# Kernel tuning notes

Measured on AMD Instinct MI355X. Metric: run time of the kernel, lower is better.

## Reference

```python
import jax, jax.numpy as jnp
import numpy as np

HIDDEN = 20


def setup_inputs() -> dict:
    key = jax.random.key(0)
    ks = jax.random.split(key, 8)
    B, T = 8192, 2048
    x = jax.random.normal(ks[0], (B, T), dtype=jnp.float32)
    # linear1: 1 -> HIDDEN
    W1 = jax.random.normal(ks[1], (HIDDEN, 1), dtype=jnp.float32) * 0.5
    b1 = jax.random.normal(ks[2], (HIDDEN,), dtype=jnp.float32) * 0.1
    # LSTMCell(HIDDEN, HIDDEN): torch layout [4*H, H], gate order i,f,g,o
    W_ih = jax.random.normal(ks[3], (4 * HIDDEN, HIDDEN), dtype=jnp.float32) * 0.2
    W_hh = jax.random.normal(ks[4], (4 * HIDDEN, HIDDEN), dtype=jnp.float32) * 0.2
    b_ih = jax.random.normal(ks[5], (4 * HIDDEN,), dtype=jnp.float32) * 0.1
    b_hh = jax.random.normal(ks[6], (4 * HIDDEN,), dtype=jnp.float32) * 0.1
    # linear2: HIDDEN -> 1
    W2 = jax.random.normal(ks[7], (1, HIDDEN), dtype=jnp.float32) * 0.2
    b2 = jnp.zeros((1,), dtype=jnp.float32)
    return {"input": x, "W1": W1, "b1": b1, "W_ih": W_ih, "W_hh": W_hh,
            "b_ih": b_ih, "b_hh": b_hh, "W2": W2, "b2": b2}


def reference(input, W1, b1, W_ih, W_hh, b_ih, b_hh, W2, b2):
    B, T = input.shape
    h0 = jnp.zeros((B, HIDDEN), dtype=input.dtype)
    c0 = jnp.zeros((B, HIDDEN), dtype=input.dtype)

    def step(carry, x_t):
        h, c = carry
        # linear1 on scalar input: [B] -> [B, HIDDEN]
        hid = x_t[:, None] * W1[:, 0][None, :] + b1
        # LSTMCell gates, torch order: i, f, g, o
        gates = hid @ W_ih.T + b_ih + h @ W_hh.T + b_hh  # [B, 4H]
        i_g, f_g, g_g, o_g = jnp.split(gates, 4, axis=-1)
        c_new = jax.nn.sigmoid(f_g) * c + jax.nn.sigmoid(i_g) * jnp.tanh(g_g)
        h_new = jax.nn.sigmoid(o_g) * jnp.tanh(c_new)
        out = h_new @ W2.T + b2  # [B, 1]
        return (h_new, c_new), out[:, 0]

    xs = input.T  # [T, B]
    _, outs = jax.lax.scan(step, (h0, c0), xs)  # outs: [T, B]
    return outs.T  # [B, T]
```

## Files before the change

kernel.cpp:

```cpp
#include <hip/hip_runtime.h>


#define HID 20
#define ROWS_PER_WAVE 3
#define NTHREADS 64
#define L2E 1.4426950408889634f

typedef float v2f __attribute__((ext_vector_type(2)));

__device__ __forceinline__ float exp2_hw(float v) { return __builtin_amdgcn_exp2f(v); }
__device__ __forceinline__ float rcp_hw(float v)  { return __builtin_amdgcn_rcpf(v); }

__device__ __forceinline__ float sig_s(float gs) {
    return rcp_hw(1.0f + exp2_hw(-gs));
}
__device__ __forceinline__ float tanh_2Ls(float gs2) {
    return (2.0f * L2E) - (4.0f * L2E) * rcp_hw(1.0f + exp2_hw(gs2));
}
__device__ __forceinline__ float tanh_c(float cs) {
    return 1.0f - 2.0f * rcp_hw(1.0f + exp2_hw(cs));
}

__global__ __attribute__((amdgpu_flat_work_group_size(NTHREADS, NTHREADS),
                          amdgpu_waves_per_eu(3, 3)))
void lstm_wave(
        const float* __restrict__ x,
        const float* __restrict__ W1,
        const float* __restrict__ b1,
        const float* __restrict__ W_ih,
        const float* __restrict__ W_hh,
        const float* __restrict__ b_ih,
        const float* __restrict__ b_hh,
        const float* __restrict__ W2,
        const float* __restrict__ b2,
        float* __restrict__ out,
        const int B, const int T)
{
    const int lane = threadIdx.x;
    const int lrow = lane / HID;
    const int m    = lane % HID;
    const bool outlane = (lrow == 3) && (m < ROWS_PER_WAVE);
    const int rslot = (lrow == 3) ? m : lrow;
    const long rowbase = (long)blockIdx.x * ROWS_PER_WAVE;
    const long row = rowbase + ((lrow == 3) ? (long)((m < 3) ? m : 0) : (long)lrow);
    const long arow = (row < B) ? row : (B - 1);
    const bool ovalid = outlane && (row < B);

    __shared__ __align__(16) float hbuf[2][ROWS_PER_WAVE + 1][HID];

    float u[4], v[4];
    if (lrow < 3) {
#pragma unroll
        for (int g = 0; g < 4; ++g) {
            const int j = g * HID + m;
            const float s = (g == 2) ? (2.0f * L2E) : L2E;
            float uu = 0.f, vv = 0.f;
#pragma unroll
            for (int k = 0; k < HID; ++k) {
                const float wi = W_ih[j * HID + k];
                uu += wi * W1[k];
                vv += wi * b1[k];
            }
            u[g] = s * uu;
            v[g] = s * (vv + b_ih[j] + b_hh[j]);
        }
    } else {
#pragma unroll
        for (int g = 0; g < 4; ++g) { u[g] = 0.f; v[g] = 0.f; }
        v[0] = b2[0];
    }

    v2f whh2[4][HID / 2];
    if (lrow < 3) {
#pragma unroll
        for (int g = 0; g < 4; ++g) {
            const int j = g * HID + m;
            const float s = (g == 2) ? (2.0f * L2E) : L2E;
#pragma unroll
            for (int kk = 0; kk < HID / 2; ++kk) {
                v2f w;
                w.x = s * W_hh[j * HID + 2 * kk];
                w.y = s * W_hh[j * HID + 2 * kk + 1];
                whh2[g][kk] = w;
            }
        }
    } else {
#pragma unroll
        for (int kk = 0; kk < HID / 2; ++kk) {
            v2f w; w.x = W2[2 * kk]; w.y = W2[2 * kk + 1];
            whh2[0][kk] = w;
            whh2[1][kk] = (v2f)(0.f);
            whh2[2][kk] = (v2f)(0.f);
            whh2[3][kk] = (v2f)(0.f);
        }
    }

#pragma unroll
    for (int g = 0; g < 4; ++g)
#pragma unroll
        for (int kk = 0; kk < HID / 2; ++kk)
            asm volatile("" : "+v"(whh2[g][kk]));

    float cs = 0.f;
    hbuf[0][lrow][m] = 0.f;
    hbuf[1][lrow][m] = 0.f;
    __syncthreads();

    const float* __restrict__ xrow = x   + arow * T;
    float* __restrict__       orow = out + arow * T;

    const float4* __restrict__ rd0 = (const float4*)&hbuf[0][rslot][0];
    const float4* __restrict__ rd1 = (const float4*)&hbuf[1][rslot][0];
    float* __restrict__ wr0 = &hbuf[1][lrow][m];
    float* __restrict__ wr1 = &hbuf[0][lrow][m];

    float xv_next = xrow[0];

#define GATE_BODY(RD, WR, OUT_IDX_VALID, OUT_IDX)                               \
    {                                                                            \
        v2f a0, a1, a2, a3;                                                      \
        a0.x = v[0] + xv * u[0]; a0.y = 0.f;                                     \
        a1.x = v[1] + xv * u[1]; a1.y = 0.f;                                     \
        a2.x = v[2] + xv * u[2]; a2.y = 0.f;                                     \
        a3.x = v[3] + xv * u[3]; a3.y = 0.f;                                     \
        _Pragma("unroll")                                                        \
        for (int q = 0; q < 5; ++q) {                                            \
            const float4 f = RD[q];                                              \
            v2f hA; hA.x = f.x; hA.y = f.y;                                      \
            v2f hB; hB.x = f.z; hB.y = f.w;                                      \
            a0 = __builtin_elementwise_fma(whh2[0][2*q],   hA, a0);              \
            a1 = __builtin_elementwise_fma(whh2[1][2*q],   hA, a1);              \
            a2 = __builtin_elementwise_fma(whh2[2][2*q],   hA, a2);              \
            a3 = __builtin_elementwise_fma(whh2[3][2*q],   hA, a3);              \
            a0 = __builtin_elementwise_fma(whh2[0][2*q+1], hB, a0);              \
            a1 = __builtin_elementwise_fma(whh2[1][2*q+1], hB, a1);              \
            a2 = __builtin_elementwise_fma(whh2[2][2*q+1], hB, a2);              \
            a3 = __builtin_elementwise_fma(whh2[3][2*q+1], hB, a3);              \
        }                                                                        \
        const float g0 = a0.x + a0.y;                                            \
        const float g1 = a1.x + a1.y;                                            \
        const float g2 = a2.x + a2.y;                                            \
        const float g3 = a3.x + a3.y;                                            \
        if ((OUT_IDX_VALID) && ovalid) orow[OUT_IDX] = g0;                       \
        const float ig  = sig_s(g0);                                             \
        const float fg  = sig_s(g1);                                             \
        const float ggs = tanh_2Ls(g2);                                          \
        const float og  = sig_s(g3);                                             \
        cs = fg * cs + ig * ggs;                                                 \
        *(WR) = og * tanh_c(cs);                                                 \
        __syncthreads();                                                         \
    }

    for (int t = 0; t < T; t += 2) {
        {
            const float xv = xv_next;
            xv_next = xrow[t + 1];
            GATE_BODY(rd0, wr0, t > 0, t - 1)
        }
        {
            const float xv = xv_next;
            const int tn = (t + 2 < T) ? (t + 2) : (T - 1);
            xv_next = xrow[tn];
            GATE_BODY(rd1, wr1, true, t)
        }
    }

    if (ovalid) {
        float o = v[0];
#pragma unroll
        for (int q = 0; q < 5; ++q) {
            const float4 f = rd0[q];
            o += whh2[0][2*q].x   * f.x + whh2[0][2*q].y   * f.y
               + whh2[0][2*q+1].x * f.z + whh2[0][2*q+1].y * f.w;
        }
        orow[T - 1] = o;
    }
#undef GATE_BODY
}

extern "C" void kernel_launch(void* const* d_in, const int* in_sizes, int n_in,
                              void* d_out, int out_size, void* d_ws, size_t ws_size,
                              hipStream_t stream) {
    (void)n_in; (void)d_ws; (void)ws_size; (void)out_size;
    const float* x    = (const float*)d_in[0];
    const float* W1   = (const float*)d_in[1];
    const float* b1   = (const float*)d_in[2];
    const float* W_ih = (const float*)d_in[3];
    const float* W_hh = (const float*)d_in[4];
    const float* b_ih = (const float*)d_in[5];
    const float* b_hh = (const float*)d_in[6];
    const float* W2   = (const float*)d_in[7];
    const float* b2   = (const float*)d_in[8];
    float* out        = (float*)d_out;

    const int B = 8192;
    const int T = in_sizes[0] / B;
    const int grid = (B + ROWS_PER_WAVE - 1) / ROWS_PER_WAVE;

    lstm_wave<<<grid, NTHREADS, 0, stream>>>(x, W1, b1, W_ih, W_hh, b_ih, b_hh, W2, b2, out, B, T);
}
```

Baseline: 1.180 ms.

## Process two independent row groups per wave to reuse W_hh registers

Each wave now advances six batch rows, two groups of three, instead of three, so every lane runs two interleaved LSTM recurrences with the same register-resident W_hh weights. This halves the grid, doubles independent FMA and transcendental work between barriers to hide latency, and spreads the per-step barrier cost over twice as many rows. The waves-per-EU hint drops from 3 to 2 to make room for the extra registers, which lowers occupancy.

After: 1.521 ms. 28.9% more time.

```diff
diff --git a/kernel.cpp b/kernel.cpp
--- a/kernel.cpp
+++ b/kernel.cpp
@@ -2,7 +2,8 @@
 
 
 #define HID 20
-#define ROWS_PER_WAVE 3
+#define RPG 3
+#define ROWS_PER_WAVE 6
 #define NTHREADS 64
 #define L2E 1.4426950408889634f
 
@@ -22,7 +23,7 @@
 }
 
 __global__ __attribute__((amdgpu_flat_work_group_size(NTHREADS, NTHREADS),
-                          amdgpu_waves_per_eu(3, 3)))
+                          amdgpu_waves_per_eu(2, 2)))
 void lstm_wave(
         const float* __restrict__ x,
         const float* __restrict__ W1,
@@ -39,17 +40,23 @@
     const int lane = threadIdx.x;
     const int lrow = lane / HID;
     const int m    = lane % HID;
-    const bool outlane = (lrow == 3) && (m < ROWS_PER_WAVE);
-    const int rslot = (lrow == 3) ? m : lrow;
+    const bool gatelane = (lane < 60);
+    const bool outlane  = (lrow == 3) && (m < RPG);
+    const int rA = gatelane ? lrow : (outlane ? m : 0);
     const long rowbase = (long)blockIdx.x * ROWS_PER_WAVE;
-    const long row = rowbase + ((lrow == 3) ? (long)((m < 3) ? m : 0) : (long)lrow);
-    const long arow = (row < B) ? row : (B - 1);
-    const bool ovalid = outlane && (row < B);
-
-    __shared__ __align__(16) float hbuf[2][ROWS_PER_WAVE + 1][HID];
+    const long rowA = rowbase + rA;
+    const long rowB = rowA + RPG;
+    const long aA = (rowA < B) ? rowA : (long)(B - 1);
+    const long aB = (rowB < B) ? rowB : (long)(B - 1);
+    const bool ovA = outlane && (rowA < B);
+    const bool ovB = outlane && (rowB < B);
+    const int rsA = gatelane ? lrow : (outlane ? m : 6);
+    const int rsB = gatelane ? (lrow + 3) : (outlane ? (m + 3) : 7);
+
+    __shared__ __align__(16) float hbuf[2][8][HID];
 
     float u[4], v[4];
-    if (lrow < 3) {
+    if (gatelane) {
 #pragma unroll
         for (int g = 0; g < 4; ++g) {
             const int j = g * HID + m;
@@ -71,7 +78,7 @@
     }
 
     v2f whh2[4][HID / 2];
-    if (lrow < 3) {
+    if (gatelane) {
 #pragma unroll
         for (int g = 0; g < 4; ++g) {
             const int j = g * HID + m;
@@ -101,81 +108,131 @@
         for (int kk = 0; kk < HID / 2; ++kk)
             asm volatile("" : "+v"(whh2[g][kk]));
 
-    float cs = 0.f;
-    hbuf[0][lrow][m] = 0.f;
-    hbuf[1][lrow][m] = 0.f;
+    float csA = 0.f, csB = 0.f;
+    if (gatelane) {
+        hbuf[0][lrow][m] = 0.f;  hbuf[0][lrow + 3][m] = 0.f;
+        hbuf[1][lrow][m] = 0.f;  hbuf[1][lrow + 3][m] = 0.f;
+    }
     __syncthreads();
 
-    const float* __restrict__ xrow = x   + arow * T;
-    float* __restrict__       orow = out + arow * T;
-
-    const float4* __restrict__ rd0 = (const float4*)&hbuf[0][rslot][0];
-    const float4* __restrict__ rd1 = (const float4*)&hbuf[1][rslot][0];
-    float* __restrict__ wr0 = &hbuf[1][lrow][m];
-    float* __restrict__ wr1 = &hbuf[0][lrow][m];
-
-    float xv_next = xrow[0];
-
-#define GATE_BODY(RD, WR, OUT_IDX_VALID, OUT_IDX)                               \
+    const float* __restrict__ xrowA = x + aA * T;
+    const float* __restrict__ xrowB = x + aB * T;
+    float* __restrict__ orowA = out + aA * T;
+    float* __restrict__ orowB = out + aB * T;
+
+    const float4* __restrict__ rdA0 = (const float4*)&hbuf[0][rsA][0];
+    const float4* __restrict__ rdA1 = (const float4*)&hbuf[1][rsA][0];
+    const float4* __restrict__ rdB0 = (const float4*)&hbuf[0][rsB][0];
+    const float4* __restrict__ rdB1 = (const float4*)&hbuf[1][rsB][0];
+    float* __restrict__ wrA0 = &hbuf[1][lrow][m];
+    float* __restrict__ wrB0 = &hbuf[1][(lrow + 3) & 7][m];
+    float* __restrict__ wrA1 = &hbuf[0][lrow][m];
+    float* __restrict__ wrB1 = &hbuf[0][(lrow + 3) & 7][m];
+
+    float xA_next = xrowA[0];
+    float xB_next = xrowB[0];
+
+#define STEP_BODY(RDA, RDB, WRA, WRB, OUTVALID_PREV, OUT_IDX)                    \
     {                                                                            \
-        v2f a0, a1, a2, a3;                                                      \
-        a0.x = v[0] + xv * u[0]; a0.y = 0.f;                                     \
-        a1.x = v[1] + xv * u[1]; a1.y = 0.f;                                     \
-        a2.x = v[2] + xv * u[2]; a2.y = 0.f;                                     \
-        a3.x = v[3] + xv * u[3]; a3.y = 0.f;                                     \
+        v2f qa0, qa1, qa2, qa3, qb0, qb1, qb2, qb3;                              \
+        qa0.x = v[0] + xA * u[0]; qa0.y = 0.f;                                   \
+        qa1.x = v[1] + xA * u[1]; qa1.y = 0.f;                                   \
+        qa2.x = v[2] + xA * u[2]; qa2.y = 0.f;                                   \
+        qa3.x = v[3] + xA * u[3]; qa3.y = 0.f;                                   \
+        qb0.x = v[0] + xB * u[0]; qb0.y = 0.f;                                   \
+        qb1.x = v[1] + xB * u[1]; qb1.y = 0.f;                                   \
+        qb2.x = v[2] + xB * u[2]; qb2.y = 0.f;                                   \
+        qb3.x = v[3] + xB * u[3]; qb3.y = 0.f;                                   \
         _Pragma("unroll")                                                        \
         for (int q = 0; q < 5; ++q) {                                            \
-            const float4 f = RD[q];                                              \
-            v2f hA; hA.x = f.x; hA.y = f.y;                                      \
-            v2f hB; hB.x = f.z; hB.y = f.w;                                      \
-            a0 = __builtin_elementwise_fma(whh2[0][2*q],   hA, a0);              \
-            a1 = __builtin_elementwise_fma(whh2[1][2*q],   hA, a1);              \
-            a2 = __builtin_elementwise_fma(whh2[2][2*q],   hA, a2);              \
-            a3 = __builtin_elementwise_fma(whh2[3][2*q],   hA, a3);              \
-            a0 = __builtin_elementwise_fma(whh2[0][2*q+1], hB, a0);              \
-            a1 = __builtin_elementwise_fma(whh2[1][2*q+1], hB, a1);              \
-            a2 = __builtin_elementwise_fma(whh2[2][2*q+1], hB, a2);              \
-            a3 = __builtin_elementwise_fma(whh2[3][2*q+1], hB, a3);              \
+            const float4 fA = RDA[q];                                            \
+            const float4 fB = RDB[q];                                            \
+            v2f hA1; hA1.x = fA.x; hA1.y = fA.y;                                 \
+            v2f hA2; hA2.x = fA.z; hA2.y = fA.w;                                 \
+            v2f hB1; hB1.x = fB.x; hB1.y = fB.y;                                 \
+            v2f hB2; hB2.x = fB.z; hB2.y = fB.w;                                 \
+            qa0 = __builtin_elementwise_fma(whh2[0][2*q],   hA1, qa0);           \
+            qb0 = __builtin_elementwise_fma(whh2[0][2*q],   hB1, qb0);           \
+            qa1 = __builtin_elementwise_fma(whh2[1][2*q],   hA1, qa1);           \
+            qb1 = __builtin_elementwise_fma(whh2[1][2*q],   hB1, qb1);           \
+            qa2 = __builtin_elementwise_fma(whh2[2][2*q],   hA1, qa2);           \
+            qb2 = __builtin_elementwise_fma(whh2[2][2*q],   hB1, qb2);           \
+            qa3 = __builtin_elementwise_fma(whh2[3][2*q],   hA1, qa3);           \
+            qb3 = __builtin_elementwise_fma(whh2[3][2*q],   hB1, qb3);           \
+            qa0 = __builtin_elementwise_fma(whh2[0][2*q+1], hA2, qa0);           \
+            qb0 = __builtin_elementwise_fma(whh2[0][2*q+1], hB2, qb0);           \
+            qa1 = __builtin_elementwise_fma(whh2[1][2*q+1], hA2, qa1);           \
+            qb1 = __builtin_elementwise_fma(whh2[1][2*q+1], hB2, qb1);           \
+            qa2 = __builtin_elementwise_fma(whh2[2][2*q+1], hA2, qa2);           \
+            qb2 = __builtin_elementwise_fma(whh2[2][2*q+1], hB2, qb2);           \
+            qa3 = __builtin_elementwise_fma(whh2[3][2*q+1], hA2, qa3);           \
+            qb3 = __builtin_elementwise_fma(whh2[3][2*q+1], hB2, qb3);           \
         }                                                                        \
-        const float g0 = a0.x + a0.y;                                            \
-        const float g1 = a1.x + a1.y;                                            \
-        const float g2 = a2.x + a2.y;                                            \
-        const float g3 = a3.x + a3.y;                                            \
-        if ((OUT_IDX_VALID) && ovalid) orow[OUT_IDX] = g0;                       \
-        const float ig  = sig_s(g0);                                             \
-        const float fg  = sig_s(g1);                                             \
-        const float ggs = tanh_2Ls(g2);                                          \
-        const float og  = sig_s(g3);                                             \
-        cs = fg * cs + ig * ggs;                                                 \
-        *(WR) = og * tanh_c(cs);                                                 \
+        const float gA0 = qa0.x + qa0.y;                                         \
+        const float gA1 = qa1.x + qa1.y;                                         \
+        const float gA2 = qa2.x + qa2.y;                                         \
+        const float gA3 = qa3.x + qa3.y;                                         \
+        const float gB0 = qb0.x + qb0.y;                                         \
+        const float gB1 = qb1.x + qb1.y;                                         \
+        const float gB2 = qb2.x + qb2.y;                                         \
+        const float gB3 = qb3.x + qb3.y;                                         \
+        if ((OUTVALID_PREV) && ovA) orowA[OUT_IDX] = gA0;                        \
+        if ((OUTVALID_PREV) && ovB) orowB[OUT_IDX] = gB0;                        \
+        const float igA  = sig_s(gA0);                                           \
+        const float igB  = sig_s(gB0);                                           \
+        const float fgA  = sig_s(gA1);                                           \
+        const float fgB  = sig_s(gB1);                                           \
+        const float ggsA = tanh_2Ls(gA2);                                        \
+        const float ggsB = tanh_2Ls(gB2);                                        \
+        const float ogA  = sig_s(gA3);                                           \
+        const float ogB  = sig_s(gB3);                                           \
+        csA = fgA * csA + igA * ggsA;                                            \
+        csB = fgB * csB + igB * ggsB;                                            \
+        const float hnA = ogA * tanh_c(csA);                                     \
+        const float hnB = ogB * tanh_c(csB);                                     \
+        if (gatelane) { *(WRA) = hnA; *(WRB) = hnB; }                            \
         __syncthreads();                                                         \
     }
 
     for (int t = 0; t < T; t += 2) {
         {
-            const float xv = xv_next;
-            xv_next = xrow[t + 1];
-            GATE_BODY(rd0, wr0, t > 0, t - 1)
+            const float xA = xA_next;
+            const float xB = xB_next;
+            xA_next = xrowA[t + 1];
+            xB_next = xrowB[t + 1];
+            STEP_BODY(rdA0, rdB0, wrA0, wrB0, t > 0, t - 1)
         }
         {
-            const float xv = xv_next;
+            const float xA = xA_next;
+            const float xB = xB_next;
             const int tn = (t + 2 < T) ? (t + 2) : (T - 1);
-            xv_next = xrow[tn];
-            GATE_BODY(rd1, wr1, true, t)
-        }
-    }
-
-    if (ovalid) {
+            xA_next = xrowA[tn];
+            xB_next = xrowB[tn];
+            STEP_BODY(rdA1, rdB1, wrA1, wrB1, true, t)
+        }
+    }
+#undef STEP_BODY
+
+    if (ovA) {
         float o = v[0];
 #pragma unroll
         for (int q = 0; q < 5; ++q) {
-            const float4 f = rd0[q];
+            const float4 f = rdA0[q];
             o += whh2[0][2*q].x   * f.x + whh2[0][2*q].y   * f.y
                + whh2[0][2*q+1].x * f.z + whh2[0][2*q+1].y * f.w;
         }
-        orow[T - 1] = o;
-    }
-#undef GATE_BODY
+        orowA[T - 1] = o;
+    }
+    if (ovB) {
+        float o = v[0];
+#pragma unroll
+        for (int q = 0; q < 5; ++q) {
+            const float4 f = rdB0[q];
+            o += whh2[0][2*q].x   * f.x + whh2[0][2*q].y   * f.y
+               + whh2[0][2*q+1].x * f.z + whh2[0][2*q+1].y * f.w;
+        }
+        orowB[T - 1] = o;
+    }
 }
 
 extern "C" void kernel_launch(void* const* d_in, const int* in_sizes, int n_in,
```
